# Performance work log

Measured on AMD Instinct MI355X. Metric: run time of the kernel, lower is better.

## Reference

```python
import jax, jax.numpy as jnp
import numpy as np

EMBED_DIM = 512
NUM_HEADS = 8
HEAD_DIM = EMBED_DIM // NUM_HEADS
EDGE_DIM = 16
B, N = 2, 2048


def setup_inputs() -> dict:
    key = jax.random.key(0)
    ks = jax.random.split(key, 16)
    s = 1.0 / np.sqrt(EMBED_DIM)
    inp = {
        "x": jax.random.normal(ks[0], (B, N, EMBED_DIM), dtype=jnp.float32),
        "adjacency": jax.random.uniform(ks[1], (B, N, N), dtype=jnp.float32),
        # torch.nn.Linear stores weight as (out, in); we keep that convention
        "Wq": jax.random.uniform(ks[2], (EMBED_DIM, EMBED_DIM), minval=-s, maxval=s),
        "bq": jax.random.uniform(ks[3], (EMBED_DIM,), minval=-s, maxval=s),
        "Wk": jax.random.uniform(ks[4], (EMBED_DIM, EMBED_DIM), minval=-s, maxval=s),
        "bk": jax.random.uniform(ks[5], (EMBED_DIM,), minval=-s, maxval=s),
        "Wv": jax.random.uniform(ks[6], (EMBED_DIM, EMBED_DIM), minval=-s, maxval=s),
        "bv": jax.random.uniform(ks[7], (EMBED_DIM,), minval=-s, maxval=s),
        "Wo": jax.random.uniform(ks[8], (EMBED_DIM, EMBED_DIM), minval=-s, maxval=s),
        "bo": jax.random.uniform(ks[9], (EMBED_DIM,), minval=-s, maxval=s),
        # edge MLP: Linear(1 -> edge_dim) then Linear(edge_dim -> num_heads)
        "We1": jax.random.uniform(ks[10], (EDGE_DIM, 1), minval=-1.0, maxval=1.0),
        "be1": jax.random.uniform(ks[11], (EDGE_DIM,), minval=-1.0, maxval=1.0),
        "We2": jax.random.uniform(ks[12], (NUM_HEADS, EDGE_DIM), minval=-0.25, maxval=0.25),
        "be2": jax.random.uniform(ks[13], (NUM_HEADS,), minval=-0.25, maxval=0.25),
        "edge_bias": jnp.zeros((NUM_HEADS,), dtype=jnp.float32),
    }
    return inp


def reference(x, adjacency, Wq, bq, Wk, bk, Wv, bv, Wo, bo, We1, be1, We2, be2, edge_bias):
    b, n, _ = x.shape
    scale = HEAD_DIM ** (-0.5)

    def split_heads(t):  # (b, n, E) -> (b, H, n, d)
        return t.reshape(b, n, NUM_HEADS, HEAD_DIM).transpose(0, 2, 1, 3)

    q = split_heads(x @ Wq.T + bq)
    k = split_heads(x @ Wk.T + bk)
    v = split_heads(x @ Wv.T + bv)

    # (b, H, n, n)
    attn_scores = jnp.einsum('bhid,bhjd->bhij', q, k) * scale

    # edge MLP applied pointwise to each adjacency entry: 1 -> edge_dim -> num_heads
    # hidden: (b, n, n, edge_dim)
    hidden = jax.nn.relu(adjacency[..., None] * We1[:, 0] + be1)
    edge_attn = jnp.einsum('bijE,hE->bhij', hidden, We2) + be2[None, :, None, None]

    boost = adjacency[:, None, :, :] * edge_bias[None, :, None, None]
    attn_scores = attn_scores + edge_attn + boost

    attn_probs = jax.nn.softmax(attn_scores, axis=-1)
    out = jnp.einsum('bhij,bhjd->bhid', attn_probs, v)
    out = out.transpose(0, 2, 1, 3).reshape(b, n, EMBED_DIM)
    out = out @ Wo.T + bo
    return out
```

## Files before the change

### kernel.cpp

```cpp
#include <hip/hip_runtime.h>
#include <stdint.h>


#define SEQ 2048
#define EMB 512
#define NH  8
#define HD  64
#define NB  2
#define L2E 1.4426950408889634f

typedef unsigned int   u32;
typedef unsigned short u16;
typedef u32   u32x4  __attribute__((ext_vector_type(4)));
typedef float f32x4  __attribute__((ext_vector_type(4)));
typedef __bf16 bf16x8 __attribute__((ext_vector_type(8)));

#define MFMA16(a, b, c) __builtin_amdgcn_mfma_f32_16x16x32_bf16((a), (b), (c), 0, 0, 0)

static __device__ __forceinline__ u16 f2bf(float f) {
  return __builtin_bit_cast(u16, (__bf16)f);
}
static __device__ __forceinline__ u32 pack2(float a, float b) {
  return (u32)f2bf(a) | ((u32)f2bf(b) << 16);
}
static __device__ __forceinline__ bf16x8 ldfrag(const u16* p) {
  return __builtin_bit_cast(bf16x8, *(const u32x4*)p);
}
static __device__ __forceinline__ void glds16(const u16* g, u16* l) {
  __builtin_amdgcn_global_load_lds(
      (const __attribute__((address_space(1))) u32*)(const void*)g,
      (__attribute__((address_space(3))) u32*)(void*)l, 16, 0, 0);
}


__global__ void prep_kernel(const float* __restrict__ x,
                            const float* __restrict__ Wq, const float* __restrict__ Wk,
                            const float* __restrict__ Wv, const float* __restrict__ Wo,
                            const float* __restrict__ We1, const float* __restrict__ be1,
                            const float* __restrict__ We2, const float* __restrict__ be2,
                            const float* __restrict__ ebias,
                            u16* __restrict__ xb, u16* __restrict__ wqkv,
                            u16* __restrict__ wob, float* __restrict__ co) {
  const int blk = blockIdx.x, tid = threadIdx.x;
  if (blk < 2048) {
    int i = (blk * 256 + tid) * 4;
    float4 v = *(const float4*)(x + i);
    *(uint2*)(xb + i) = make_uint2(pack2(v.x, v.y), pack2(v.z, v.w));
  } else if (blk < 3072) {
    int i = ((blk - 2048) * 256 + tid) * 4;
    int m = i >> 18;
    int off = i & 262143;
    const float* src = (m == 0) ? Wq : ((m == 1) ? Wk : ((m == 2) ? Wv : Wo));
    u16* dst = (m < 3) ? (wqkv + (size_t)m * 262144) : wob;
    float4 v = *(const float4*)(src + off);
    *(uint2*)(dst + off) = make_uint2(pack2(v.x, v.y), pack2(v.z, v.w));
  } else {
    const int e = tid & 15, h = tid >> 4;
    if (tid < 128) {
      co[49 + e * 8 + h] = 0.0f;
      if (h == 0) { co[17 + e] = 0.0f; co[33 + e] = 0.0f; }
    }
    __syncthreads();
    if (tid < 128) {
      float w1 = We1[e], b1 = be1[e], w2 = We2[h * 16 + e];
      float u0 = b1, u1 = w1 + b1;
      bool on  = (u0 >= 0.0f) && (u1 >= 0.0f);
      bool off = (u0 <= 0.0f) && (u1 <= 0.0f);
      bool crossing = (!on) && (!off);
      float ca = on ? (w2 * b1) : (crossing ? 0.5f * w2 * b1 : 0.0f);
      float cb = on ? (w2 * w1) : (crossing ? 0.5f * w2 * w1 : 0.0f);
      #pragma unroll
      for (int d = 1; d < 16; d <<= 1) { ca += __shfl_xor(ca, d); cb += __shfl_xor(cb, d); }
      if (e == 0) { co[h] = (be2[h] + ca) * L2E; co[8 + h] = (ebias[h] + cb) * L2E; }
      unsigned long long msk = __ballot(crossing);
      int midx = __popcll(msk & 0xFFFFull & ((1ull << e) - 1ull));
      int mcnt = __popcll(msk & 0xFFFFull);
      if (crossing) {
        co[49 + midx * 8 + h] = 0.5f * w2 * L2E;
        if (h == 0) { co[17 + midx] = w1; co[33 + midx] = b1; }
      }
      if (tid == 0) ((int*)co)[16] = mcnt;
    }
  }
}

#define LDA 40
__global__ __launch_bounds__(256) void gemm_qkv_kernel(
    const u16* __restrict__ A, const u16* __restrict__ Bm,
    const float* __restrict__ bq, const float* __restrict__ bk, const float* __restrict__ bv,
    u16* __restrict__ qh, u16* __restrict__ ksw, u16* __restrict__ vsw)
{
  __shared__ u16 sm[64 * LDA + 128 * LDA];
  u16* As = sm;
  u16* Bs = sm + 64 * LDA;
  const int tid = threadIdx.x;
  const int lane = tid & 63, w = tid >> 6;
  const int q = lane >> 4, l15 = lane & 15;
  const int m0 = blockIdx.y * 64;
  const int n0 = blockIdx.x * 128;

  f32x4 acc[4][2];
  f32x4 zero = {0.f, 0.f, 0.f, 0.f};
  #pragma unroll
  for (int i = 0; i < 4; i++) { acc[i][0] = zero; acc[i][1] = zero; }

  const bool isA = tid < 128;
  const int arow_ = tid >> 1, ahalf = tid & 1;
  const int brow = tid - 128;
  const u16* ga = A  + (size_t)(m0 + arow_) * EMB + ahalf * 16;
  const u16* gb = Bm + (size_t)(n0 + brow) * EMB;
  u16* la = &As[arow_ * LDA + ahalf * 16];
  u16* lb = &Bs[brow * LDA];

  u32x4 p0, p1, p2, p3;
  if (isA) {
    p0 = *(const u32x4*)(ga); p1 = *(const u32x4*)(ga + 8); ga += 32;
  } else {
    p0 = *(const u32x4*)(gb);      p1 = *(const u32x4*)(gb + 8);
    p2 = *(const u32x4*)(gb + 16); p3 = *(const u32x4*)(gb + 24); gb += 32;
  }

  for (int k0 = 0; k0 < EMB; k0 += 32) {
    __syncthreads();
    if (isA) { *(u32x4*)(la) = p0; *(u32x4*)(la + 8) = p1; }
    else {
      *(u32x4*)(lb)      = p0; *(u32x4*)(lb + 8)  = p1;
      *(u32x4*)(lb + 16) = p2; *(u32x4*)(lb + 24) = p3;
    }
    __syncthreads();
    if (k0 + 32 < EMB) {
      if (isA) { p0 = *(const u32x4*)(ga); p1 = *(const u32x4*)(ga + 8); ga += 32; }
      else {
        p0 = *(const u32x4*)(gb);      p1 = *(const u32x4*)(gb + 8);
        p2 = *(const u32x4*)(gb + 16); p3 = *(const u32x4*)(gb + 24); gb += 32;
      }
    }
    bf16x8 af[4], bfr[2];
    #pragma unroll
    for (int mi = 0; mi < 4; mi++)
      af[mi] = ldfrag(&As[(mi*16 + l15) * LDA + q*8]);
    #pragma unroll
    for (int ni = 0; ni < 2; ni++)
      bfr[ni] = ldfrag(&Bs[(w*32 + ni*16 + l15) * LDA + q*8]);
    #pragma unroll
    for (int mi = 0; mi < 4; mi++)
      #pragma unroll
      for (int ni = 0; ni < 2; ni++)
        acc[mi][ni] = MFMA16(af[mi], bfr[ni], acc[mi][ni]);
  }

  const int mat = n0 >> 9;
  const float* bias = (mat == 0) ? bq : ((mat == 1) ? bk : bv);
  const float mul = (mat == 0) ? 0.125f * L2E : 1.0f;
  const int b_ = m0 >> 11;
  const int nbase = m0 & 2047;

  #pragma unroll
  for (int p = 0; p < 2; p++) {
    __syncthreads();
    if ((w >> 1) == p) {
      #pragma unroll
      for (int ni = 0; ni < 2; ni++) {
        const int dd = (w & 1) * 32 + ni * 16 + l15;
        const float bsv = bias[(n0 & 511) + (w * 32 + ni * 16 + l15)];
        #pragma unroll
        for (int mi = 0; mi < 4; mi++) {
          #pragma unroll
          for (int r = 0; r < 4; r++) {
            const int nr = mi * 16 + q * 4 + r;
            const float val = (acc[mi][ni][r] + bsv) * mul;
            int idx;
            if (mat == 0)      idx = nr * 64 + dd;
            else if (mat == 1) idx = (nr >> 4) * 1024 + ((dd >> 5) << 9)
                                   + ((((dd >> 3) & 3) * 16 + (nr & 15)) << 3) + (dd & 7);
            else               idx = ((dd >> 4) << 10) + (((nr >> 5) & 1) << 9)
                                   + ((((nr >> 3) & 3) * 16 + (dd & 15)) << 3) + (nr & 7);
            sm[idx] = f2bf(val);
          }
        }
      }
    }
    __syncthreads();
    const int hh = ((n0 & 511) >> 6) + p;
    u16* gdst;
    if (mat == 0)      gdst = qh  + ((size_t)(b_ * NH + hh) * SEQ + nbase) * HD;
    else if (mat == 1) gdst = ksw + (size_t)(b_ * NH + hh) * 131072 + (nbase >> 4) * 1024;
    else               gdst = vsw + (size_t)(b_ * NH + hh) * 131072 + (nbase >> 6) * 4096;
    *(u32x4*)(gdst + tid * 16)     = *(const u32x4*)(sm + tid * 16);
    *(u32x4*)(gdst + tid * 16 + 8) = *(const u32x4*)(sm + tid * 16 + 8);
  }
}

__global__ __launch_bounds__(256) void gemm_out_kernel(
    const u16* __restrict__ A, const u16* __restrict__ Bm,
    const float* __restrict__ bo, float* __restrict__ out)
{
  __shared__ u16 As[64 * LDA];
  __shared__ u16 Bs[64 * LDA];
  const int tid = threadIdx.x;
  const int lane = tid & 63, w = tid >> 6;
  const int q = lane >> 4, l15 = lane & 15;
  const int m0 = blockIdx.y * 64;
  const int n0 = blockIdx.x * 64;

  f32x4 acc[4];
  f32x4 zero = {0.f, 0.f, 0.f, 0.f};
  #pragma unroll
  for (int i = 0; i < 4; i++) acc[i] = zero;

  const bool isA = tid < 128;
  const int row = isA ? (tid >> 1) : ((tid - 128) >> 1);
  const int half = tid & 1;
  const u16* g = (isA ? A + (size_t)(m0 + row) * EMB : Bm + (size_t)(n0 + row) * EMB)
               + half * 16;
  u16* l = (isA ? &As[row * LDA] : &Bs[row * LDA]) + half * 16;

  u32x4 p0 = *(const u32x4*)(g);
  u32x4 p1 = *(const u32x4*)(g + 8);
  g += 32;

  for (int k0 = 0; k0 < EMB; k0 += 32) {
    __syncthreads();
    *(u32x4*)(l) = p0; *(u32x4*)(l + 8) = p1;
    __syncthreads();
    if (k0 + 32 < EMB) {
      p0 = *(const u32x4*)(g); p1 = *(const u32x4*)(g + 8); g += 32;
    }
    bf16x8 af[4], bfr;
    #pragma unroll
    for (int mi = 0; mi < 4; mi++)
      af[mi] = ldfrag(&As[(mi*16 + l15) * LDA + q*8]);
    bfr = ldfrag(&Bs[(w*16 + l15) * LDA + q*8]);
    #pragma unroll
    for (int mi = 0; mi < 4; mi++)
      acc[mi] = MFMA16(af[mi], bfr, acc[mi]);
  }

  int col = n0 + w*16 + l15;
  float bsv = bo[col];
  #pragma unroll
  for (int mi = 0; mi < 4; mi++) {
    int rowb = m0 + mi*16 + q*4;
    #pragma unroll
    for (int r = 0; r < 4; r++)
      out[(size_t)(rowb + r) * EMB + col] = acc[mi][r] + bsv;
  }
}

template<int MT>
struct FlashCtx {
  const u16 *kgp, *vgp;
  const float* arow;
  bf16x8 qf0, qf1;
  float Ah, Bh;
  float ctr[MT], dtr[MT], wtr[MT];
  int lane, w, q, l15, pxor;
};

template<int MT>
static __device__ __forceinline__ void flash_stage(const FlashCtx<MT>& c,
                                                   u16* Kb, u16* Vb, int it) {
  const int o = c.w * 1024 + c.lane * 8;
  const u16* kg = c.kgp + it * 4096;
  const u16* vg = c.vgp + it * 4096;
  glds16(kg + o,       Kb + o);
  glds16(kg + o + 512, Kb + o + 512);
  glds16(vg + o,       Vb + o);
  glds16(vg + o + 512, Vb + o + 512);
}

template<int MT>
static __device__ __forceinline__ void flash_iter(
    const FlashCtx<MT>& c, int it, int tend, u16* Kb, u16* Vb, u16* nKb, u16* nVb,
    u16* psw, float4* avc, float4* avn, f32x4* O, float& lsum)
{
  __syncthreads();
  if (it + 1 < tend) flash_stage(c, nKb, nVb, it + 1);
  const int nx = (it + 1 < tend) ? it + 1 : tend - 1;
  #pragma unroll
  for (int jt = 0; jt < 4; jt++)
    avn[jt] = *(const float4*)(c.arow + nx * 64 + jt * 16);
  __builtin_amdgcn_sched_barrier(0);

  f32x4 zero = {0.f, 0.f, 0.f, 0.f};
  const int lo = c.lane * 8;

  f32x4 S[4];
  #pragma unroll
  for (int jt = 0; jt < 4; jt++) {
    bf16x8 kf0 = ldfrag(Kb + jt * 1024 + lo);
    bf16x8 kf1 = ldfrag(Kb + jt * 1024 + 512 + lo);
    f32x4 s = MFMA16(kf0, c.qf0, zero);
    S[jt] = MFMA16(kf1, c.qf1, s);
  }

  #pragma unroll
  for (int half = 0; half < 2; half++) {
    #pragma unroll
    for (int jj = 0; jj < 2; jj++) {
      const int jt = half * 2 + jj;
      float p[4];
      #pragma unroll
      for (int r = 0; r < 4; r++) {
        float a = ((const float*)&avc[jt])[r];
        float e = fmaf(a, c.Bh, c.Ah);
        #pragma unroll
        for (int t = 0; t < MT; t++)
          e = fmaf(fabsf(fmaf(a, c.ctr[t], c.dtr[t])), c.wtr[t], e);
        p[r] = __builtin_amdgcn_exp2f(S[jt][r] + e);
        lsum += p[r];
      }
      *(uint2*)(psw + ((c.l15 * 64 + jt * 16 + c.q * 4) ^ c.pxor)) =
          make_uint2(pack2(p[0], p[1]), pack2(p[2], p[3]));
    }
    bf16x8 pf = ldfrag(psw + ((c.l15 * 64 + half * 32 + c.q * 8) ^ c.pxor));
    #pragma unroll
    for (int dt = 0; dt < 4; dt++) {
      bf16x8 vf = ldfrag(Vb + dt * 1024 + half * 512 + lo);
      O[dt] = MFMA16(vf, pf, O[dt]);
    }
  }
}

template<int MT>
__device__ __forceinline__ void flash_body(
    u16* Kb0, u16* Kb1, u16* Vb0, u16* Vb1, u16* Pb,
    const u16* __restrict__ qh, const u16* __restrict__ ksw, const u16* __restrict__ vsw,
    const float* __restrict__ adj, const float* __restrict__ coeff,
    u16* __restrict__ om0, u16* __restrict__ om1, float* __restrict__ lsp)
{
  const int tid = threadIdx.x, lane = tid & 63, w = tid >> 6;
  const int q = lane >> 4, l15 = lane & 15;
  const int i0 = blockIdx.x * 64;
  const int h = blockIdx.y;
  const int b = blockIdx.z >> 1, jh = blockIdx.z & 1;
  const int t0 = jh * 16, tend = t0 + 16;
  const int bh = b * NH + h;
  const int iw = i0 + w * 16;

  FlashCtx<MT> c;
  c.lane = lane; c.w = w; c.q = q; c.l15 = l15;
  c.pxor = (l15 & 7) << 3;
  c.Ah = coeff[h]; c.Bh = coeff[8 + h];
  #pragma unroll
  for (int t = 0; t < MT; t++) {
    c.ctr[t] = coeff[17 + t];
    c.dtr[t] = coeff[33 + t];
    c.wtr[t] = coeff[49 + t * 8 + h];
  }
  const u16* qrow = qh + ((size_t)bh * SEQ + iw + l15) * HD;
  c.qf0 = ldfrag(qrow + q * 8);
  c.qf1 = ldfrag(qrow + 32 + q * 8);
  c.kgp = ksw + (size_t)bh * 131072;
  c.vgp = vsw + (size_t)bh * 131072;
  c.arow = adj + ((size_t)b * SEQ + iw + l15) * SEQ + q * 4;

  f32x4 O[4];
  f32x4 zero = {0.f, 0.f, 0.f, 0.f};
  #pragma unroll
  for (int dt = 0; dt < 4; dt++) O[dt] = zero;
  float lsum = 0.0f;

  u16* psw = Pb + w * 1024;

  flash_stage(c, Kb0, Vb0, t0);
  float4 avA[4], avB[4];
  #pragma unroll
  for (int jt = 0; jt < 4; jt++)
    avA[jt] = *(const float4*)(c.arow + t0 * 64 + jt * 16);

  #pragma unroll 1
  for (int it2 = t0; it2 < tend; it2 += 2) {
    flash_iter(c, it2,     tend, Kb0, Vb0, Kb1, Vb1, psw, avA, avB, O, lsum);
    flash_iter(c, it2 + 1, tend, Kb1, Vb1, Kb0, Vb0, psw, avB, avA, O, lsum);
  }

  lsum += __shfl_xor(lsum, 16);
  lsum += __shfl_xor(lsum, 32);
  if (lane < 16)
    lsp[(size_t)jh * 32768 + (size_t)bh * SEQ + iw + l15] = lsum;

  u16* orow = (jh ? om1 : om0)
            + ((size_t)b * SEQ + iw + l15) * EMB + h * HD + q * 4;
  #pragma unroll
  for (int dt = 0; dt < 4; dt++)
    *(uint2*)(orow + dt * 16) = make_uint2(pack2(O[dt][0], O[dt][1]),
                                           pack2(O[dt][2], O[dt][3]));
}

__global__ __launch_bounds__(256, 4) void flash_kernel(
    const u16* __restrict__ qh, const u16* __restrict__ ksw, const u16* __restrict__ vsw,
    const float* __restrict__ adj, const float* __restrict__ coeff,
    u16* __restrict__ om0, u16* __restrict__ om1, float* __restrict__ lsp)
{
  __shared__ __align__(16) u16 Kb[2][4096];
  __shared__ __align__(16) u16 Vb[2][4096];
  __shared__ __align__(16) u16 Pb[4096];
  const int mt = ((const int*)coeff)[16];
  if (mt <= 4)
    flash_body<4>(Kb[0], Kb[1], Vb[0], Vb[1], Pb, qh, ksw, vsw, adj, coeff, om0, om1, lsp);
  else if (mt <= 8)
    flash_body<8>(Kb[0], Kb[1], Vb[0], Vb[1], Pb, qh, ksw, vsw, adj, coeff, om0, om1, lsp);
  else
    flash_body<16>(Kb[0], Kb[1], Vb[0], Vb[1], Pb, qh, ksw, vsw, adj, coeff, om0, om1, lsp);
}

__global__ __launch_bounds__(256) void combine_kernel(
    u16* __restrict__ om0, const u16* __restrict__ om1,
    const float* __restrict__ lsp)
{
  const int g = blockIdx.x * 256 + threadIdx.x;
  const int idx = g * 4;
  const int row = idx >> 9;
  const int h = (idx >> 6) & 7;
  const int li = ((row >> 11) * NH + h) * SEQ + (row & 2047);
  const float rl = 1.0f / (lsp[li] + lsp[32768 + li]);
  uint2 a = *(const uint2*)(om0 + idx);
  uint2 d = *(const uint2*)(om1 + idx);
  const float o0 = __builtin_bit_cast(float, a.x << 16)
                 + __builtin_bit_cast(float, d.x << 16);
  const float o1 = __builtin_bit_cast(float, a.x & 0xffff0000u)
                 + __builtin_bit_cast(float, d.x & 0xffff0000u);
  const float o2 = __builtin_bit_cast(float, a.y << 16)
                 + __builtin_bit_cast(float, d.y << 16);
  const float o3 = __builtin_bit_cast(float, a.y & 0xffff0000u)
                 + __builtin_bit_cast(float, d.y & 0xffff0000u);
  *(uint2*)(om0 + idx) = make_uint2(pack2(o0 * rl, o1 * rl),
                                    pack2(o2 * rl, o3 * rl));
}

extern "C" void kernel_launch(void* const* d_in, const int* in_sizes, int n_in,
                              void* d_out, int out_size, void* d_ws, size_t ws_size,
                              hipStream_t stream) {
  const float* x     = (const float*)d_in[0];
  const float* adj   = (const float*)d_in[1];
  const float* Wq    = (const float*)d_in[2];
  const float* bq    = (const float*)d_in[3];
  const float* Wk    = (const float*)d_in[4];
  const float* bk    = (const float*)d_in[5];
  const float* Wv    = (const float*)d_in[6];
  const float* bv    = (const float*)d_in[7];
  const float* Wo    = (const float*)d_in[8];
  const float* bo    = (const float*)d_in[9];
  const float* We1   = (const float*)d_in[10];
  const float* be1   = (const float*)d_in[11];
  const float* We2   = (const float*)d_in[12];
  const float* be2   = (const float*)d_in[13];
  const float* ebias = (const float*)d_in[14];
  float* out = (float*)d_out;

  char* ws = (char*)d_ws;
  u16*   xb   = (u16*)(ws + 0);
  u16*   wqkv = (u16*)(ws + 4194304);
  u16*   wob  = (u16*)(ws + 5767168);
  u16*   qh   = (u16*)(ws + 6291456);
  u16*   ksw  = (u16*)(ws + 10485760);
  u16*   vsw  = (u16*)(ws + 14680064);
  u16*   om0  = (u16*)(ws + 18874368);
  float* co   = (float*)(ws + 23068672);
  u16*   om1  = xb;
  float* lsp  = (float*)wqkv;
  if (ws_size < 23069696) return;

  prep_kernel<<<3073, 256, 0, stream>>>(x, Wq, Wk, Wv, Wo, We1, be1, We2, be2, ebias,
                                        xb, wqkv, wob, co);
  gemm_qkv_kernel<<<dim3(12, 64), 256, 0, stream>>>(xb, wqkv, bq, bk, bv, qh, ksw, vsw);
  flash_kernel<<<dim3(32, NH, NB * 2), 256, 0, stream>>>(qh, ksw, vsw, adj, co,
                                                         om0, om1, lsp);
  combine_kernel<<<2048, 256, 0, stream>>>(om0, om1, lsp);
  gemm_out_kernel<<<dim3(8, 64), 256, 0, stream>>>(om0, wob, bo, out);
}
```

Baseline: 191.3 us.

## Fuse split-KV combine into output GEMM and widen GEMM K-step to 64

Removes the separate combine kernel and instead merges the two split-KV partial outputs, normalised by the summed row sums, while staging the A tile in the output projection GEMM. Both GEMMs now advance K by 64 per iteration with a wider LDS row stride, halving the number of barrier pairs and loop iterations. This drops one launch plus a full read-modify-write pass over the attention output, at the cost of recomputing the combine per N-tile (8x redundant reads of om0/om1) and more registers per thread.

```diff
diff --git a/kernel.cpp b/kernel.cpp
--- a/kernel.cpp
+++ b/kernel.cpp
@@ -30,6 +30,19 @@
   __builtin_amdgcn_global_load_lds(
       (const __attribute__((address_space(1))) u32*)(const void*)g,
       (__attribute__((address_space(3))) u32*)(void*)l, 16, 0, 0);
+}
+static __device__ __forceinline__ u32 comb2(u32 a, u32 d, float rl) {
+  float lo = __builtin_bit_cast(float, a << 16)
+           + __builtin_bit_cast(float, d << 16);
+  float hi = __builtin_bit_cast(float, a & 0xffff0000u)
+           + __builtin_bit_cast(float, d & 0xffff0000u);
+  return pack2(lo * rl, hi * rl);
+}
+static __device__ __forceinline__ u32x4 comb4(u32x4 a, u32x4 d, float rl) {
+  u32x4 r;
+  r[0] = comb2(a[0], d[0], rl); r[1] = comb2(a[1], d[1], rl);
+  r[2] = comb2(a[2], d[2], rl); r[3] = comb2(a[3], d[3], rl);
+  return r;
 }
 
 
@@ -84,15 +97,15 @@
   }
 }
 
-#define LDA 40
+#define LDB 72
 __global__ __launch_bounds__(256) void gemm_qkv_kernel(
     const u16* __restrict__ A, const u16* __restrict__ Bm,
     const float* __restrict__ bq, const float* __restrict__ bk, const float* __restrict__ bv,
     u16* __restrict__ qh, u16* __restrict__ ksw, u16* __restrict__ vsw)
 {
-  __shared__ u16 sm[64 * LDA + 128 * LDA];
+  __shared__ u16 sm[64 * LDB + 128 * LDB];
   u16* As = sm;
-  u16* Bs = sm + 64 * LDA;
+  u16* Bs = sm + 64 * LDB;
   const int tid = threadIdx.x;
   const int lane = tid & 63, w = tid >> 6;
   const int q = lane >> 4, l15 = lane & 15;
@@ -104,49 +117,49 @@
   #pragma unroll
   for (int i = 0; i < 4; i++) { acc[i][0] = zero; acc[i][1] = zero; }
 
-  const bool isA = tid < 128;
-  const int arow_ = tid >> 1, ahalf = tid & 1;
-  const int brow = tid - 128;
-  const u16* ga = A  + (size_t)(m0 + arow_) * EMB + ahalf * 16;
-  const u16* gb = Bm + (size_t)(n0 + brow) * EMB;
-  u16* la = &As[arow_ * LDA + ahalf * 16];
-  u16* lb = &Bs[brow * LDA];
-
-  u32x4 p0, p1, p2, p3;
-  if (isA) {
-    p0 = *(const u32x4*)(ga); p1 = *(const u32x4*)(ga + 8); ga += 32;
-  } else {
-    p0 = *(const u32x4*)(gb);      p1 = *(const u32x4*)(gb + 8);
-    p2 = *(const u32x4*)(gb + 16); p3 = *(const u32x4*)(gb + 24); gb += 32;
-  }
-
-  for (int k0 = 0; k0 < EMB; k0 += 32) {
-    __syncthreads();
-    if (isA) { *(u32x4*)(la) = p0; *(u32x4*)(la + 8) = p1; }
-    else {
-      *(u32x4*)(lb)      = p0; *(u32x4*)(lb + 8)  = p1;
-      *(u32x4*)(lb + 16) = p2; *(u32x4*)(lb + 24) = p3;
-    }
-    __syncthreads();
-    if (k0 + 32 < EMB) {
-      if (isA) { p0 = *(const u32x4*)(ga); p1 = *(const u32x4*)(ga + 8); ga += 32; }
-      else {
-        p0 = *(const u32x4*)(gb);      p1 = *(const u32x4*)(gb + 8);
-        p2 = *(const u32x4*)(gb + 16); p3 = *(const u32x4*)(gb + 24); gb += 32;
-      }
-    }
-    bf16x8 af[4], bfr[2];
+  const int ar = tid >> 2, aq = tid & 3;
+  const int br = tid >> 1, bh = tid & 1;
+  const u16* ga = A  + (size_t)(m0 + ar) * EMB + aq * 16;
+  const u16* gb = Bm + (size_t)(n0 + br) * EMB + bh * 32;
+  u16* la = &As[ar * LDB + aq * 16];
+  u16* lb = &Bs[br * LDB + bh * 32];
+
+  u32x4 a0, a1, b0, b1, b2, b3;
+  a0 = *(const u32x4*)(ga);      a1 = *(const u32x4*)(ga + 8);
+  b0 = *(const u32x4*)(gb);      b1 = *(const u32x4*)(gb + 8);
+  b2 = *(const u32x4*)(gb + 16); b3 = *(const u32x4*)(gb + 24);
+  ga += 64; gb += 64;
+
+  for (int k0 = 0; k0 < EMB; k0 += 64) {
+    __syncthreads();
+    *(u32x4*)(la) = a0;      *(u32x4*)(la + 8) = a1;
+    *(u32x4*)(lb) = b0;      *(u32x4*)(lb + 8) = b1;
+    *(u32x4*)(lb + 16) = b2; *(u32x4*)(lb + 24) = b3;
+    __syncthreads();
+    if (k0 + 64 < EMB) {
+      a0 = *(const u32x4*)(ga);      a1 = *(const u32x4*)(ga + 8);
+      b0 = *(const u32x4*)(gb);      b1 = *(const u32x4*)(gb + 8);
+      b2 = *(const u32x4*)(gb + 16); b3 = *(const u32x4*)(gb + 24);
+      ga += 64; gb += 64;
+    }
+    bf16x8 af[4][2], bfr[2][2];
     #pragma unroll
     for (int mi = 0; mi < 4; mi++)
-      af[mi] = ldfrag(&As[(mi*16 + l15) * LDA + q*8]);
+      #pragma unroll
+      for (int kk = 0; kk < 2; kk++)
+        af[mi][kk] = ldfrag(&As[(mi*16 + l15) * LDB + kk*32 + q*8]);
     #pragma unroll
     for (int ni = 0; ni < 2; ni++)
-      bfr[ni] = ldfrag(&Bs[(w*32 + ni*16 + l15) * LDA + q*8]);
+      #pragma unroll
+      for (int kk = 0; kk < 2; kk++)
+        bfr[ni][kk] = ldfrag(&Bs[(w*32 + ni*16 + l15) * LDB + kk*32 + q*8]);
     #pragma unroll
     for (int mi = 0; mi < 4; mi++)
       #pragma unroll
       for (int ni = 0; ni < 2; ni++)
-        acc[mi][ni] = MFMA16(af[mi], bfr[ni], acc[mi][ni]);
+        #pragma unroll
+        for (int kk = 0; kk < 2; kk++)
+          acc[mi][ni] = MFMA16(af[mi][kk], bfr[ni][kk], acc[mi][ni]);
   }
 
   const int mat = n0 >> 9;
@@ -192,11 +205,12 @@
 }
 
 __global__ __launch_bounds__(256) void gemm_out_kernel(
-    const u16* __restrict__ A, const u16* __restrict__ Bm,
+    const u16* __restrict__ om0, const u16* __restrict__ om1,
+    const float* __restrict__ lsp, const u16* __restrict__ Bm,
     const float* __restrict__ bo, float* __restrict__ out)
 {
-  __shared__ u16 As[64 * LDA];
-  __shared__ u16 Bs[64 * LDA];
+  __shared__ u16 As[64 * LDB];
+  __shared__ u16 Bs[64 * LDB];
   const int tid = threadIdx.x;
   const int lane = tid & 63, w = tid >> 6;
   const int q = lane >> 4, l15 = lane & 15;
@@ -208,32 +222,51 @@
   #pragma unroll
   for (int i = 0; i < 4; i++) acc[i] = zero;
 
-  const bool isA = tid < 128;
-  const int row = isA ? (tid >> 1) : ((tid - 128) >> 1);
-  const int half = tid & 1;
-  const u16* g = (isA ? A + (size_t)(m0 + row) * EMB : Bm + (size_t)(n0 + row) * EMB)
-               + half * 16;
-  u16* l = (isA ? &As[row * LDA] : &Bs[row * LDA]) + half * 16;
-
-  u32x4 p0 = *(const u32x4*)(g);
-  u32x4 p1 = *(const u32x4*)(g + 8);
-  g += 32;
-
-  for (int k0 = 0; k0 < EMB; k0 += 32) {
-    __syncthreads();
-    *(u32x4*)(l) = p0; *(u32x4*)(l + 8) = p1;
-    __syncthreads();
-    if (k0 + 32 < EMB) {
-      p0 = *(const u32x4*)(g); p1 = *(const u32x4*)(g + 8); g += 32;
-    }
-    bf16x8 af[4], bfr;
+  const int ar = tid >> 2, aq = tid & 3;
+  const int arow = m0 + ar;
+  const int libase = (arow >> 11) * 16384 + (arow & 2047);
+  const u16* ga0 = om0 + (size_t)arow * EMB + aq * 16;
+  const u16* ga1 = om1 + (size_t)arow * EMB + aq * 16;
+  const u16* gb  = Bm + (size_t)(n0 + ar) * EMB + aq * 16;
+  u16* la = &As[ar * LDB + aq * 16];
+  u16* lb = &Bs[ar * LDB + aq * 16];
+
+  u32x4 a0, a1, d0, d1, b0, b1;
+  float rl;
+  a0 = *(const u32x4*)(ga0); a1 = *(const u32x4*)(ga0 + 8);
+  d0 = *(const u32x4*)(ga1); d1 = *(const u32x4*)(ga1 + 8);
+  b0 = *(const u32x4*)(gb);  b1 = *(const u32x4*)(gb + 8);
+  rl = 1.0f / (lsp[libase] + lsp[32768 + libase]);
+  ga0 += 64; ga1 += 64; gb += 64;
+
+  for (int k0 = 0; k0 < EMB; k0 += 64) {
+    __syncthreads();
+    *(u32x4*)(la)     = comb4(a0, d0, rl);
+    *(u32x4*)(la + 8) = comb4(a1, d1, rl);
+    *(u32x4*)(lb) = b0; *(u32x4*)(lb + 8) = b1;
+    __syncthreads();
+    if (k0 + 64 < EMB) {
+      const int h = (k0 + 64) >> 6;
+      a0 = *(const u32x4*)(ga0); a1 = *(const u32x4*)(ga0 + 8);
+      d0 = *(const u32x4*)(ga1); d1 = *(const u32x4*)(ga1 + 8);
+      b0 = *(const u32x4*)(gb);  b1 = *(const u32x4*)(gb + 8);
+      rl = 1.0f / (lsp[libase + h * 2048] + lsp[32768 + libase + h * 2048]);
+      ga0 += 64; ga1 += 64; gb += 64;
+    }
+    bf16x8 af[4][2], bfr[2];
     #pragma unroll
     for (int mi = 0; mi < 4; mi++)
-      af[mi] = ldfrag(&As[(mi*16 + l15) * LDA + q*8]);
-    bfr = ldfrag(&Bs[(w*16 + l15) * LDA + q*8]);
+      #pragma unroll
+      for (int kk = 0; kk < 2; kk++)
+        af[mi][kk] = ldfrag(&As[(mi*16 + l15) * LDB + kk*32 + q*8]);
+    #pragma unroll
+    for (int kk = 0; kk < 2; kk++)
+      bfr[kk] = ldfrag(&Bs[(w*16 + l15) * LDB + kk*32 + q*8]);
     #pragma unroll
     for (int mi = 0; mi < 4; mi++)
-      acc[mi] = MFMA16(af[mi], bfr, acc[mi]);
+      #pragma unroll
+      for (int kk = 0; kk < 2; kk++)
+        acc[mi] = MFMA16(af[mi][kk], bfr[kk], acc[mi]);
   }
 
   int col = n0 + w*16 + l15;
@@ -403,30 +436,6 @@
     flash_body<8>(Kb[0], Kb[1], Vb[0], Vb[1], Pb, qh, ksw, vsw, adj, coeff, om0, om1, lsp);
   else
     flash_body<16>(Kb[0], Kb[1], Vb[0], Vb[1], Pb, qh, ksw, vsw, adj, coeff, om0, om1, lsp);
-}
-
-__global__ __launch_bounds__(256) void combine_kernel(
-    u16* __restrict__ om0, const u16* __restrict__ om1,
-    const float* __restrict__ lsp)
-{
-  const int g = blockIdx.x * 256 + threadIdx.x;
-  const int idx = g * 4;
-  const int row = idx >> 9;
-  const int h = (idx >> 6) & 7;
-  const int li = ((row >> 11) * NH + h) * SEQ + (row & 2047);
-  const float rl = 1.0f / (lsp[li] + lsp[32768 + li]);
-  uint2 a = *(const uint2*)(om0 + idx);
-  uint2 d = *(const uint2*)(om1 + idx);
-  const float o0 = __builtin_bit_cast(float, a.x << 16)
-                 + __builtin_bit_cast(float, d.x << 16);
-  const float o1 = __builtin_bit_cast(float, a.x & 0xffff0000u)
-                 + __builtin_bit_cast(float, d.x & 0xffff0000u);
-  const float o2 = __builtin_bit_cast(float, a.y << 16)
-                 + __builtin_bit_cast(float, d.y << 16);
-  const float o3 = __builtin_bit_cast(float, a.y & 0xffff0000u)
-                 + __builtin_bit_cast(float, d.y & 0xffff0000u);
-  *(uint2*)(om0 + idx) = make_uint2(pack2(o0 * rl, o1 * rl),
-                                    pack2(o2 * rl, o3 * rl));
 }
 
 extern "C" void kernel_launch(void* const* d_in, const int* in_sizes, int n_in,
@@ -467,6 +476,5 @@
   gemm_qkv_kernel<<<dim3(12, 64), 256, 0, stream>>>(xb, wqkv, bq, bk, bv, qh, ksw, vsw);
   flash_kernel<<<dim3(32, NH, NB * 2), 256, 0, stream>>>(qh, ksw, vsw, adj, co,
                                                          om0, om1, lsp);
-  combine_kernel<<<2048, 256, 0, stream>>>(om0, om1, lsp);
-  gemm_out_kernel<<<dim3(8, 64), 256, 0, stream>>>(om0, wob, bo, out);
-}
+  gemm_out_kernel<<<dim3(8, 64), 256, 0, stream>>>(om0, om1, lsp, wob, bo, out);
+}
```

After: 185.2 us. -3.2%, faster.
